# Performance work log

Hardware: AMD Instinct MI355X
Metric: run time of the kernel (lower is better)

## Reference

```python
import jax, jax.numpy as jnp
import numpy as np
from jax import lax

NUM_LAYERS = 4
EPS_BN = 1e-5
EPS_AGG = 1e-6


def _bn(x, gamma, beta):
    # training-mode batch norm over the leading (node/edge) dim
    m = x.mean(axis=0)
    v = x.var(axis=0)
    return gamma * (x - m) / jnp.sqrt(v + EPS_BN) + beta


def setup_inputs() -> dict:
    key = jax.random.key(0)
    ks = jax.random.split(key, 32)
    N, E, D, L, K = 50000, 400000, 64, 128, 16
    s = 0.05
    inp = {
        'reads': jax.random.uniform(ks[0], (N, 4, L), jnp.float32),
        'src': jax.random.randint(ks[1], (E,), 0, N, jnp.int32),
        'dst': jax.random.randint(ks[2], (E,), 0, N, jnp.int32),
        'overlap_similarity': jax.random.uniform(ks[3], (E,), jnp.float32),
        'overlap_length': jax.random.normal(ks[4], (E,), jnp.float32),
        # sequence encoder conv: Conv1d(4 -> D, kernel K)
        'conv_w': jax.random.normal(ks[5], (D, 4, K), jnp.float32) * s,
        'conv_b': jnp.zeros((D,), jnp.float32),
        # edge encoder: Linear(2 -> D)
        'We': jax.random.normal(ks[6], (2, D), jnp.float32) * s,
        'be': jnp.zeros((D,), jnp.float32),
        # GatedGCN per-layer weights, stacked on leading layer dim
        'A1': jax.random.normal(ks[7], (NUM_LAYERS, D, D), jnp.float32) * s,
        'A2': jax.random.normal(ks[8], (NUM_LAYERS, D, D), jnp.float32) * s,
        'A3': jax.random.normal(ks[9], (NUM_LAYERS, D, D), jnp.float32) * s,
        'bA1': jnp.zeros((NUM_LAYERS, D), jnp.float32),
        'bA2': jnp.zeros((NUM_LAYERS, D), jnp.float32),
        'bA3': jnp.zeros((NUM_LAYERS, D), jnp.float32),
        'U': jax.random.normal(ks[10], (NUM_LAYERS, D, D), jnp.float32) * s,
        'V': jax.random.normal(ks[11], (NUM_LAYERS, D, D), jnp.float32) * s,
        'bU': jnp.zeros((NUM_LAYERS, D), jnp.float32),
        'bV': jnp.zeros((NUM_LAYERS, D), jnp.float32),
        'bn_h_gamma': jnp.ones((NUM_LAYERS, D), jnp.float32),
        'bn_h_beta': jnp.zeros((NUM_LAYERS, D), jnp.float32),
        'bn_e_gamma': jnp.ones((NUM_LAYERS, D), jnp.float32),
        'bn_e_beta': jnp.zeros((NUM_LAYERS, D), jnp.float32),
        # edge decoder MLP: Linear(3D -> D) -> ReLU -> Linear(D -> 1)
        'W1': jax.random.normal(ks[12], (3 * D, D), jnp.float32) * s,
        'b1': jnp.zeros((D,), jnp.float32),
        'W2': jax.random.normal(ks[13], (D, 1), jnp.float32) * s,
        'b2': jnp.zeros((1,), jnp.float32),
    }
    return inp


def reference(reads, src, dst, overlap_similarity, overlap_length,
              conv_w, conv_b, We, be,
              A1, A2, A3, bA1, bA2, bA3, U, V, bU, bV,
              bn_h_gamma, bn_h_beta, bn_e_gamma, bn_e_beta,
              W1, b1, W2, b2):
    N = reads.shape[0]
    # --- SequenceEncoder: Conv1d over one-hot reads, global max-pool ---
    hseq = lax.conv_general_dilated(
        reads, conv_w, window_strides=(1,), padding='VALID',
        dimension_numbers=('NCH', 'OIH', 'NCH'))  # [N, D, L-K+1]
    h = (hseq + conv_b[None, :, None]).max(axis=2)  # [N, D]
    # --- EdgeEncoder: Linear on [similarity, length] ---
    e = jnp.stack([overlap_similarity, overlap_length], axis=1) @ We + be  # [E, D]
    # --- stacked GatedGCN layers (gather src/dst, scatter-aggregate to dst) ---
    for l in range(NUM_LAYERS):
        hs = h[src]  # [E, D] gather
        hd = h[dst]
        e_hat = (hs @ A1[l] + bA1[l]) + (hd @ A2[l] + bA2[l]) + (e @ A3[l] + bA3[l])
        sigma = jax.nn.sigmoid(e_hat)  # edge gates
        Vh = hs @ V[l] + bV[l]
        num = jax.ops.segment_sum(sigma * Vh, dst, num_segments=N)  # [N, D]
        den = jax.ops.segment_sum(sigma, dst, num_segments=N)
        h_hat = (h @ U[l] + bU[l]) + num / (den + EPS_AGG)
        h = h + jax.nn.relu(_bn(h_hat, bn_h_gamma[l], bn_h_beta[l]))
        e = e + jax.nn.relu(_bn(e_hat, bn_e_gamma[l], bn_e_beta[l]))
    # --- EdgeDecoder: MLP on [h_src, h_dst, e] ---
    z = jnp.concatenate([h[src], h[dst], e], axis=1)  # [E, 3D]
    p = jax.nn.relu(z @ W1 + b1) @ W2 + b2  # [E, 1]
    return p
```

## Files before the change

### kernel.cpp

```cpp
#include <hip/hip_runtime.h>
#include <hip/hip_bf16.h>
#include <cstdint>
#include <cstddef>

#define DD 64

typedef __attribute__((ext_vector_type(8))) short short8;
typedef __attribute__((ext_vector_type(4))) float f32x4;

__device__ __forceinline__ float4 f4_0() { return make_float4(0.f, 0.f, 0.f, 0.f); }

__device__ __forceinline__ unsigned short f2bf(float f) {
  __hip_bfloat16 h = __float2bfloat16(f);
  return *reinterpret_cast<unsigned short*>(&h);
}
__device__ __forceinline__ float bfl(unsigned u) { return __uint_as_float(u << 16); }
__device__ __forceinline__ float bfh(unsigned u) { return __uint_as_float(u & 0xffff0000u); }
__device__ __forceinline__ float b2f(unsigned short u) {
  return __uint_as_float(((unsigned)u) << 16);
}

__device__ __forceinline__ short8 pack_bf16x8(float4 a, float4 b) {
  union { unsigned short us[8]; short8 v; } pk;
  pk.us[0] = f2bf(a.x); pk.us[1] = f2bf(a.y); pk.us[2] = f2bf(a.z); pk.us[3] = f2bf(a.w);
  pk.us[4] = f2bf(b.x); pk.us[5] = f2bf(b.y); pk.us[6] = f2bf(b.z); pk.us[7] = f2bf(b.w);
  return pk.v;
}

__device__ __forceinline__ short8 lds_frag(const unsigned short* p) {
  uint2 lo = *reinterpret_cast<const uint2*>(p);
  uint2 hi = *reinterpret_cast<const uint2*>(p + 4);
  union { unsigned u[4]; short8 v; } t;
  t.u[0] = lo.x; t.u[1] = lo.y; t.u[2] = hi.x; t.u[3] = hi.y;
  return t.v;
}
__device__ __forceinline__ short8 g_frag(const unsigned short* p) {
  return *reinterpret_cast<const short8*>(p);
}
__device__ __forceinline__ short8 u4_to_s8(uint4 v) {
  union { uint4 u; short8 s; } t; t.u = v; return t.s;
}

__global__ __launch_bounds__(256) void k_hist(const int* __restrict__ dst,
                                              int* __restrict__ cnt, int E) {
  int j = blockIdx.x * 256 + threadIdx.x;
  if (j < E) atomicAdd(&cnt[dst[j]], 1);
}

__global__ __launch_bounds__(1024) void k_scan(const int* __restrict__ cnt,
                                               int* __restrict__ row_ptr,
                                               int* __restrict__ nxt, int N, int E) {
  __shared__ int wsum[16];
  __shared__ int carry_s;
  const int tid = threadIdx.x;
  const int wid = tid >> 6, lane = tid & 63;
  if (tid == 0) carry_s = 0;
  __syncthreads();
  const int ntl = (N + 4095) / 4096;
  for (int b = 0; b < ntl; ++b) {
    const int i0 = b * 4096 + tid * 4;
    int v0 = 0, v1 = 0, v2 = 0, v3 = 0;
    if (i0 + 3 < N) {
      int4 q = *reinterpret_cast<const int4*>(cnt + i0);
      v0 = q.x; v1 = q.y; v2 = q.z; v3 = q.w;
    } else {
      if (i0 < N) v0 = cnt[i0];
      if (i0 + 1 < N) v1 = cnt[i0 + 1];
      if (i0 + 2 < N) v2 = cnt[i0 + 2];
      if (i0 + 3 < N) v3 = cnt[i0 + 3];
    }
    const int tsum = v0 + v1 + v2 + v3;
    int x = tsum;
#pragma unroll
    for (int off = 1; off < 64; off <<= 1) {
      int y = __shfl_up(x, off, 64);
      if (lane >= off) x += y;
    }
    if (lane == 63) wsum[wid] = x;
    __syncthreads();
    if (wid == 0 && lane < 16) {
      int wv = wsum[lane];
#pragma unroll
      for (int off = 1; off < 16; off <<= 1) {
        int y = __shfl_up(wv, off, 64);
        if (lane >= off) wv += y;
      }
      wsum[lane] = wv;
    }
    __syncthreads();
    int base = carry_s + (wid > 0 ? wsum[wid - 1] : 0) + (x - tsum);
    int e1 = base + v0, e2 = e1 + v1, e3 = e2 + v2;
    if (i0 < N) { row_ptr[i0] = base; nxt[i0] = base; }
    if (i0 + 1 < N) { row_ptr[i0 + 1] = e1; nxt[i0 + 1] = e1; }
    if (i0 + 2 < N) { row_ptr[i0 + 2] = e2; nxt[i0 + 2] = e2; }
    if (i0 + 3 < N) { row_ptr[i0 + 3] = e3; nxt[i0 + 3] = e3; }
    __syncthreads();
    if (tid == 0) carry_s += wsum[15];
    __syncthreads();
  }
  if (tid == 0) row_ptr[N] = E;
}

__global__ __launch_bounds__(256) void k_scatter(const int* __restrict__ dst,
                                                 const int* __restrict__ src,
                                                 int* __restrict__ nxt,
                                                 int* __restrict__ order,
                                                 int* __restrict__ psrc,
                                                 int2* __restrict__ pedge, int E) {
  int j = blockIdx.x * 256 + threadIdx.x;
  if (j >= E) return;
  int d = dst[j];
  int s = src[j];
  int pos = atomicAdd(&nxt[d], 1);
  order[pos] = j;
  psrc[pos] = s;
  pedge[pos] = make_int2(s, d);
}

__global__ __launch_bounds__(256) void k_prep(const float* __restrict__ A1,
                                              const float* __restrict__ A2,
                                              const float* __restrict__ V,
                                              const float* __restrict__ U,
                                              const float* __restrict__ A3,
                                              const float* __restrict__ W1,
                                              unsigned short* __restrict__ T) {
  const int b = blockIdx.x;
  const int tid = threadIdx.x;
  if (b < 20) {
    const int l = b / 5, m = b % 5;
    const float* srcp =
        (m == 0 ? A1 : m == 1 ? A2 : m == 2 ? V : m == 3 ? U : A3) + l * 4096;
    unsigned short* dstp = T + b * 4096;
    for (int i = tid; i < 4096; i += 256) {
      int n = i >> 6, k = i & 63;
      dstp[i] = f2bf(srcp[k * 64 + n]);
    }
  } else {
    unsigned short* dstp = T + 20 * 4096;
    for (int i = tid; i < 12288; i += 256) {
      int n = i / 192, k = i % 192;
      dstp[i] = f2bf(W1[k * 64 + n]);
    }
  }
}

struct ConvRegs { float4 v[3][2]; };

__device__ __forceinline__ void conv_load(const float* __restrict__ reads, int N,
                                          int g, int tid, ConvRegs& R) {
#pragma unroll
  for (int it = 0; it < 3; ++it) {
    const int task = tid + it * 256;
    R.v[it][0] = f4_0(); R.v[it][1] = f4_0();
    if (task < 576) {
      const int node = task / 144, rem = task % 144;
      const int c = rem / 36, u = rem % 36;
      const int gn = g * 4 + node;
      if (gn < N) {
        const float* rp = reads + (size_t)gn * 512 + c * 128 + 4 * u;
        if (u <= 31) R.v[it][0] = *reinterpret_cast<const float4*>(rp);
        if (u <= 30) R.v[it][1] = *reinterpret_cast<const float4*>(rp + 4);
      }
    }
  }
}

__device__ __forceinline__ void conv_write(unsigned short* __restrict__ cbuf,
                                           int tid, const ConvRegs& R) {
#pragma unroll
  for (int it = 0; it < 3; ++it) {
    const int task = tid + it * 256;
    if (task < 576) {
      const int node = task / 144, rem = task % 144;
      const int c = rem / 36, u = rem % 36;
      const float4 v0 = R.v[it][0], v1 = R.v[it][1];
      unsigned pk0, pk1, pk2, pk3;
      asm("v_cvt_pk_bf16_f32 %0, %1, %2" : "=v"(pk0) : "v"(v0.x), "v"(v0.y));
      asm("v_cvt_pk_bf16_f32 %0, %1, %2" : "=v"(pk1) : "v"(v0.z), "v"(v0.w));
      asm("v_cvt_pk_bf16_f32 %0, %1, %2" : "=v"(pk2) : "v"(v1.x), "v"(v1.y));
      asm("v_cvt_pk_bf16_f32 %0, %1, %2" : "=v"(pk3) : "v"(v1.z), "v"(v1.w));
      const unsigned a0 = __builtin_amdgcn_alignbit(pk1, pk0, 16);
      const unsigned a1 = __builtin_amdgcn_alignbit(pk2, pk1, 16);
      const unsigned a2 = __builtin_amdgcn_alignbit(pk3, pk2, 16);
      const int base = ((node * 4 + c) * 4) * 144 + 4 * u;
      *reinterpret_cast<uint2*>(&cbuf[base + 0 * 144]) = make_uint2(pk0, pk1);
      *reinterpret_cast<uint2*>(&cbuf[base + 1 * 144]) = make_uint2(a0, a1);
      *reinterpret_cast<uint2*>(&cbuf[base + 2 * 144]) = make_uint2(pk1, pk2);
      *reinterpret_cast<uint2*>(&cbuf[base + 3 * 144]) = make_uint2(a1, a2);
    }
  }
}

__global__ __launch_bounds__(256) void k_conv_mfma(const float* __restrict__ reads,
                                                   const float* __restrict__ w,
                                                   const float* __restrict__ bias,
                                                   float* __restrict__ h, int N) {
  __shared__ unsigned short cp[2][4 * 4 * 4 * 144];
  const int tid = threadIdx.x;
  const int wid = tid >> 6, lane = tid & 63;
  const int col = lane & 15, grp = lane >> 4;
  const int ngroups = (N + 3) / 4;
  if ((int)blockIdx.x >= ngroups) return;
  short8 wf[4][2];
#pragma unroll
  for (int nt = 0; nt < 4; ++nt)
#pragma unroll
    for (int ks = 0; ks < 2; ++ks) {
      const int d = nt * 16 + col;
      const int kb = ks * 32 + grp * 8;
      const float* wp = w + d * 64 + kb;
      float4 w0 = *reinterpret_cast<const float4*>(wp);
      float4 w1 = *reinterpret_cast<const float4*>(wp + 4);
      wf[nt][ks] = pack_bf16x8(w0, w1);
    }
  ConvRegs RA, RB;
  conv_load(reads, N, blockIdx.x, tid, RA);
  int p = 0;
  const int s = col & 3;
  for (int g = blockIdx.x; g < ngroups; g += gridDim.x) {
    conv_write(&cp[p][0], tid, RA);
    const int gnext = g + gridDim.x;
    if (gnext < ngroups) conv_load(reads, N, gnext, tid, RB);
    __syncthreads();
    const int gn = g * 4 + wid;
    if (gn < N) {
      const unsigned short* cbuf = &cp[p][0];
      float vmax[4];
#pragma unroll
      for (int nt = 0; nt < 4; ++nt) vmax[nt] = -3.0e38f;
      for (int mt = 0; mt < 8; ++mt) {
        const int t = mt * 16 + col;
        short8 af[2];
#pragma unroll
        for (int ks = 0; ks < 2; ++ks) {
          const int kbase = ks * 32 + grp * 8;
          const int c = kbase >> 4;
          const int kk0 = kbase & 15;
          const int q = (t - s) + kk0;
          af[ks] = lds_frag(&cbuf[((wid * 4 + c) * 4 + s) * 144 + q]);
        }
        f32x4 acc[4] = {};
#pragma unroll
        for (int ks = 0; ks < 2; ++ks)
#pragma unroll
          for (int nt = 0; nt < 4; ++nt)
            acc[nt] = __builtin_amdgcn_mfma_f32_16x16x32_bf16(af[ks], wf[nt][ks], acc[nt], 0, 0, 0);
        if (mt < 7) {
#pragma unroll
          for (int nt = 0; nt < 4; ++nt)
#pragma unroll
            for (int r = 0; r < 4; ++r) vmax[nt] = fmaxf(vmax[nt], acc[nt][r]);
        } else {
          if (grp == 0) {
#pragma unroll
            for (int nt = 0; nt < 4; ++nt) vmax[nt] = fmaxf(vmax[nt], acc[nt][0]);
          }
        }
      }
#pragma unroll
      for (int off = 16; off <= 32; off <<= 1)
#pragma unroll
        for (int nt = 0; nt < 4; ++nt)
          vmax[nt] = fmaxf(vmax[nt], __shfl_xor(vmax[nt], off, 64));
      if (grp == 0) {
#pragma unroll
        for (int nt = 0; nt < 4; ++nt) {
          const int d = nt * 16 + col;
          h[(size_t)gn * 64 + d] = vmax[nt] + bias[d];
        }
      }
    }
    p ^= 1;
    RA = RB;
  }
}

__global__ __launch_bounds__(256) void k_node_mfma(const float* __restrict__ h_in,
                                                   float* __restrict__ h_out,
                                                   const float* __restrict__ hhat,
                                                   const float* __restrict__ sums_prev,
                                                   const float* __restrict__ gam,
                                                   const float* __restrict__ bet,
                                                   const unsigned short* __restrict__ Wt4,
                                                   const float* __restrict__ bA1,
                                                   const float* __restrict__ bA2,
                                                   const float* __restrict__ bV,
                                                   const float* __restrict__ bU,
                                                   unsigned short* __restrict__ XA1,
                                                   unsigned short* __restrict__ XA2,
                                                   unsigned short* __restrict__ XV,
                                                   float* __restrict__ XU,
                                                   int N, int hasupd) {
  __shared__ float s_coef[128];
  const int tid = threadIdx.x;
  if (hasupd) {
    if (tid < 64) {
      const float invR = 1.f / (float)N;
      float mean = sums_prev[tid] * invR;
      float var = sums_prev[64 + tid] * invR - mean * mean;
      float sc = gam[tid] * rsqrtf(var + 1e-5f);
      s_coef[tid] = sc;
      s_coef[64 + tid] = bet[tid] - mean * sc;
    }
    __syncthreads();
  }
  const int wid = tid >> 6, lane = tid & 63;
  const int col = lane & 15, g = lane >> 4;
  const int ntiles = (N + 15) / 16;
  for (int tw = blockIdx.x * 4 + wid; tw < ntiles; tw += gridDim.x * 4) {
    int n = tw * 16 + col;
    const bool valid = n < N;
    if (!valid) n = N - 1;
    short8 bfr[2];
#pragma unroll
    for (int ks = 0; ks < 2; ++ks) {
      const int c0 = ks * 32 + g * 8;
      const float* hp = h_in + (size_t)n * 64 + c0;
      float4 x0 = *reinterpret_cast<const float4*>(hp);
      float4 x1 = *reinterpret_cast<const float4*>(hp + 4);
      if (hasupd) {
        const float* yp = hhat + (size_t)n * 64 + c0;
        float4 y0 = *reinterpret_cast<const float4*>(yp);
        float4 y1 = *reinterpret_cast<const float4*>(yp + 4);
        float4 sc0 = *reinterpret_cast<const float4*>(&s_coef[c0]);
        float4 sc1 = *reinterpret_cast<const float4*>(&s_coef[c0 + 4]);
        float4 sh0 = *reinterpret_cast<const float4*>(&s_coef[64 + c0]);
        float4 sh1 = *reinterpret_cast<const float4*>(&s_coef[64 + c0 + 4]);
        x0.x += fmaxf(fmaf(sc0.x, y0.x, sh0.x), 0.f);
        x0.y += fmaxf(fmaf(sc0.y, y0.y, sh0.y), 0.f);
        x0.z += fmaxf(fmaf(sc0.z, y0.z, sh0.z), 0.f);
        x0.w += fmaxf(fmaf(sc0.w, y0.w, sh0.w), 0.f);
        x1.x += fmaxf(fmaf(sc1.x, y1.x, sh1.x), 0.f);
        x1.y += fmaxf(fmaf(sc1.y, y1.y, sh1.y), 0.f);
        x1.z += fmaxf(fmaf(sc1.z, y1.z, sh1.z), 0.f);
        x1.w += fmaxf(fmaf(sc1.w, y1.w, sh1.w), 0.f);
        if (valid) {
          float* op = h_out + (size_t)n * 64 + c0;
          *reinterpret_cast<float4*>(op) = x0;
          *reinterpret_cast<float4*>(op + 4) = x1;
        }
      }
      bfr[ks] = pack_bf16x8(x0, x1);
    }
#pragma unroll
    for (int m = 0; m < 4; ++m) {
      const unsigned short* Wm = Wt4 + m * 4096;
      f32x4 acc[4] = {};
#pragma unroll
      for (int ks = 0; ks < 2; ++ks) {
        const int ko = ks * 32 + g * 8;
#pragma unroll
        for (int mt = 0; mt < 4; ++mt) {
          short8 aa = g_frag(Wm + (mt * 16 + col) * 64 + ko);
          acc[mt] = __builtin_amdgcn_mfma_f32_16x16x32_bf16(aa, bfr[ks], acc[mt], 0, 0, 0);
        }
      }
      if (!valid) continue;
      const float* bb = (m == 0) ? bA1 : (m == 1) ? bA2 : (m == 2) ? bV : bU;
#pragma unroll
      for (int mt = 0; mt < 4; ++mt) {
        const int chb = mt * 16 + g * 4;
        float4 bv = *reinterpret_cast<const float4*>(bb + chb);
        float o0 = acc[mt][0] + bv.x;
        float o1 = acc[mt][1] + bv.y;
        float o2 = acc[mt][2] + bv.z;
        float o3 = acc[mt][3] + bv.w;
        if (m < 3) {
          unsigned short* X = (m == 0) ? XA1 : (m == 1) ? XA2 : XV;
          ushort4 ov;
          ov.x = f2bf(o0); ov.y = f2bf(o1); ov.z = f2bf(o2); ov.w = f2bf(o3);
          *reinterpret_cast<ushort4*>(X + (size_t)n * 64 + chb) = ov;
        } else {
          *reinterpret_cast<float4*>(XU + (size_t)n * 64 + chb) =
              make_float4(o0, o1, o2, o3);
        }
      }
    }
  }
}

__global__ __launch_bounds__(256) void k_edge_mfma0(unsigned short* __restrict__ e,
                                                    unsigned short* __restrict__ ehat_out,
                                                    const float* __restrict__ sim,
                                                    const float* __restrict__ olen,
                                                    const int* __restrict__ order,
                                                    const float* __restrict__ We,
                                                    const float* __restrict__ be,
                                                    const int2* __restrict__ pedge,
                                                    const unsigned short* __restrict__ XA1,
                                                    const unsigned short* __restrict__ XA2,
                                                    const unsigned short* __restrict__ A3t,
                                                    const float* __restrict__ bA3,
                                                    float* __restrict__ sums_out, int E) {
  __shared__ float s_sums[128];
  const int tid = threadIdx.x;
  if (tid < 128) s_sums[tid] = 0.f;
  __syncthreads();
  const int wid = tid >> 6, lane = tid & 63;
  const int col = lane & 15, g = lane >> 4;
  float4 ba[4];
#pragma unroll
  for (int mt = 0; mt < 4; ++mt)
    ba[mt] = *reinterpret_cast<const float4*>(bA3 + mt * 16 + g * 4);
  float4 w0[2][2], w1[2][2], bev[2][2];
#pragma unroll
  for (int ks = 0; ks < 2; ++ks) {
    const int c0 = ks * 32 + g * 8;
    w0[ks][0] = *reinterpret_cast<const float4*>(We + c0);
    w0[ks][1] = *reinterpret_cast<const float4*>(We + c0 + 4);
    w1[ks][0] = *reinterpret_cast<const float4*>(We + 64 + c0);
    w1[ks][1] = *reinterpret_cast<const float4*>(We + 64 + c0 + 4);
    bev[ks][0] = *reinterpret_cast<const float4*>(be + c0);
    bev[ks][1] = *reinterpret_cast<const float4*>(be + c0 + 4);
  }
  float statS[16], statQ[16];
#pragma unroll
  for (int i = 0; i < 16; ++i) { statS[i] = 0.f; statQ[i] = 0.f; }
  const int ntiles = (E + 15) / 16;
  const int stride = gridDim.x * 4;
  int tw = blockIdx.x * 4 + wid;
  int2 idx_n = make_int2(0, 0);
  int oe_n = 0;
  if (tw < ntiles) {
    int p = tw * 16 + col; if (p >= E) p = E - 1;
    idx_n = pedge[p];
    oe_n = order[p];
  }
  for (; tw < ntiles; tw += stride) {
    int p = tw * 16 + col;
    const bool valid = p < E;
    if (!valid) p = E - 1;
    const int se = idx_n.x, de = idx_n.y;
    const float sv = sim[oe_n], lv = olen[oe_n];
    ushort4 gx1[4], gx2[4];
#pragma unroll
    for (int mt = 0; mt < 4; ++mt) {
      const int chb = mt * 16 + g * 4;
      gx1[mt] = *reinterpret_cast<const ushort4*>(XA1 + (size_t)se * 64 + chb);
      gx2[mt] = *reinterpret_cast<const ushort4*>(XA2 + (size_t)de * 64 + chb);
    }
    const int twn = tw + stride;
    if (twn < ntiles) {
      int pn = twn * 16 + col; if (pn >= E) pn = E - 1;
      idx_n = pedge[pn];
      oe_n = order[pn];
    }
    short8 bfr[2];
#pragma unroll
    for (int ks = 0; ks < 2; ++ks) {
      float4 e0, e1;
      e0.x = fmaf(sv, w0[ks][0].x, fmaf(lv, w1[ks][0].x, bev[ks][0].x));
      e0.y = fmaf(sv, w0[ks][0].y, fmaf(lv, w1[ks][0].y, bev[ks][0].y));
      e0.z = fmaf(sv, w0[ks][0].z, fmaf(lv, w1[ks][0].z, bev[ks][0].z));
      e0.w = fmaf(sv, w0[ks][0].w, fmaf(lv, w1[ks][0].w, bev[ks][0].w));
      e1.x = fmaf(sv, w0[ks][1].x, fmaf(lv, w1[ks][1].x, bev[ks][1].x));
      e1.y = fmaf(sv, w0[ks][1].y, fmaf(lv, w1[ks][1].y, bev[ks][1].y));
      e1.z = fmaf(sv, w0[ks][1].z, fmaf(lv, w1[ks][1].z, bev[ks][1].z));
      e1.w = fmaf(sv, w0[ks][1].w, fmaf(lv, w1[ks][1].w, bev[ks][1].w));
      bfr[ks] = pack_bf16x8(e0, e1);
      if (valid)
        *reinterpret_cast<short8*>(e + (size_t)p * 64 + ks * 32 + g * 8) = bfr[ks];
    }
    f32x4 acc[4] = {};
#pragma unroll
    for (int ks = 0; ks < 2; ++ks)
#pragma unroll
      for (int mt = 0; mt < 4; ++mt) {
        short8 aa = g_frag(A3t + (mt * 16 + col) * 64 + ks * 32 + g * 8);
        acc[mt] = __builtin_amdgcn_mfma_f32_16x16x32_bf16(aa, bfr[ks], acc[mt], 0, 0, 0);
      }
    if (valid) {
#pragma unroll
      for (int mt = 0; mt < 4; ++mt) {
        const int chb = mt * 16 + g * 4;
        float o0 = acc[mt][0] + b2f(gx1[mt].x) + b2f(gx2[mt].x) + ba[mt].x;
        float o1 = acc[mt][1] + b2f(gx1[mt].y) + b2f(gx2[mt].y) + ba[mt].y;
        float o2 = acc[mt][2] + b2f(gx1[mt].z) + b2f(gx2[mt].z) + ba[mt].z;
        float o3 = acc[mt][3] + b2f(gx1[mt].w) + b2f(gx2[mt].w) + ba[mt].w;
        ushort4 ov;
        ov.x = f2bf(o0); ov.y = f2bf(o1); ov.z = f2bf(o2); ov.w = f2bf(o3);
        *reinterpret_cast<ushort4*>(ehat_out + (size_t)p * 64 + chb) = ov;
        statS[mt * 4 + 0] += o0; statQ[mt * 4 + 0] = fmaf(o0, o0, statQ[mt * 4 + 0]);
        statS[mt * 4 + 1] += o1; statQ[mt * 4 + 1] = fmaf(o1, o1, statQ[mt * 4 + 1]);
        statS[mt * 4 + 2] += o2; statQ[mt * 4 + 2] = fmaf(o2, o2, statQ[mt * 4 + 2]);
        statS[mt * 4 + 3] += o3; statQ[mt * 4 + 3] = fmaf(o3, o3, statQ[mt * 4 + 3]);
      }
    }
  }
#pragma unroll
  for (int off = 1; off <= 8; off <<= 1)
#pragma unroll
    for (int i = 0; i < 16; ++i) {
      statS[i] += __shfl_xor(statS[i], off, 64);
      statQ[i] += __shfl_xor(statQ[i], off, 64);
    }
  if (col == 0) {
#pragma unroll
    for (int mt = 0; mt < 4; ++mt)
#pragma unroll
      for (int c = 0; c < 4; ++c) {
        const int ch = mt * 16 + g * 4 + c;
        atomicAdd(&s_sums[ch], statS[mt * 4 + c]);
        atomicAdd(&s_sums[64 + ch], statQ[mt * 4 + c]);
      }
  }
  __syncthreads();
  if (tid < 128) atomicAdd(&sums_out[tid], s_sums[tid]);
}

__global__ __launch_bounds__(256) void k_edge_mfma(unsigned short* __restrict__ e,
                                                   const unsigned short* __restrict__ ehat_prev,
                                                   unsigned short* __restrict__ ehat_out,
                                                   const float* __restrict__ sums_prev,
                                                   const float* __restrict__ gprev,
                                                   const float* __restrict__ bprev,
                                                   const int2* __restrict__ pedge,
                                                   const unsigned short* __restrict__ XA1,
                                                   const unsigned short* __restrict__ XA2,
                                                   const unsigned short* __restrict__ A3t,
                                                   const float* __restrict__ bA3,
                                                   float* __restrict__ sums_out, int E) {
  __shared__ float s_coef[128];
  __shared__ float s_sums[128];
  const int tid = threadIdx.x;
  if (tid < 128) s_sums[tid] = 0.f;
  if (tid < 64) {
    float mean = sums_prev[tid] / (float)E;
    float var = sums_prev[64 + tid] / (float)E - mean * mean;
    float sc = gprev[tid] * rsqrtf(var + 1e-5f);
    s_coef[tid] = sc;
    s_coef[64 + tid] = bprev[tid] - mean * sc;
  }
  __syncthreads();
  const int wid = tid >> 6, lane = tid & 63;
  const int col = lane & 15, g = lane >> 4;
  float4 ba[4];
#pragma unroll
  for (int mt = 0; mt < 4; ++mt)
    ba[mt] = *reinterpret_cast<const float4*>(bA3 + mt * 16 + g * 4);
  float statS[16], statQ[16];
#pragma unroll
  for (int i = 0; i < 16; ++i) { statS[i] = 0.f; statQ[i] = 0.f; }
  const int ntiles = (E + 15) / 16;
  const int stride = gridDim.x * 4;
  int tw = blockIdx.x * 4 + wid;
  int2 idx_n = make_int2(0, 0);
  uint4 eo_n0, eo_n1, hv_n0, hv_n1;
  if (tw < ntiles) {
    int p = tw * 16 + col; if (p >= E) p = E - 1;
    idx_n = pedge[p];
    const unsigned short* ep = e + (size_t)p * 64 + g * 8;
    eo_n0 = *reinterpret_cast<const uint4*>(ep);
    eo_n1 = *reinterpret_cast<const uint4*>(ep + 32);
    const unsigned short* hp = ehat_prev + (size_t)p * 64 + g * 8;
    hv_n0 = *reinterpret_cast<const uint4*>(hp);
    hv_n1 = *reinterpret_cast<const uint4*>(hp + 32);
  }
  for (; tw < ntiles; tw += stride) {
    int p = tw * 16 + col;
    const bool valid = p < E;
    if (!valid) p = E - 1;
    const int se = idx_n.x, de = idx_n.y;
    const uint4 eoc[2] = {eo_n0, eo_n1};
    const uint4 hvc[2] = {hv_n0, hv_n1};
    ushort4 gx1[4], gx2[4];
#pragma unroll
    for (int mt = 0; mt < 4; ++mt) {
      const int chb = mt * 16 + g * 4;
      gx1[mt] = *reinterpret_cast<const ushort4*>(XA1 + (size_t)se * 64 + chb);
      gx2[mt] = *reinterpret_cast<const ushort4*>(XA2 + (size_t)de * 64 + chb);
    }
    const int twn = tw + stride;
    if (twn < ntiles) {
      int pn = twn * 16 + col; if (pn >= E) pn = E - 1;
      idx_n = pedge[pn];
      const unsigned short* ep = e + (size_t)pn * 64 + g * 8;
      eo_n0 = *reinterpret_cast<const uint4*>(ep);
      eo_n1 = *reinterpret_cast<const uint4*>(ep + 32);
      const unsigned short* hp = ehat_prev + (size_t)pn * 64 + g * 8;
      hv_n0 = *reinterpret_cast<const uint4*>(hp);
      hv_n1 = *reinterpret_cast<const uint4*>(hp + 32);
    }
    short8 bfr[2];
#pragma unroll
    for (int ks = 0; ks < 2; ++ks) {
      const int c0 = ks * 32 + g * 8;
      const uint4 eo = eoc[ks];
      const uint4 hv = hvc[ks];
      float4 e0 = make_float4(bfl(eo.x), bfh(eo.x), bfl(eo.y), bfh(eo.y));
      float4 e1 = make_float4(bfl(eo.z), bfh(eo.z), bfl(eo.w), bfh(eo.w));
      float4 sc0 = *reinterpret_cast<const float4*>(&s_coef[c0]);
      float4 sc1 = *reinterpret_cast<const float4*>(&s_coef[c0 + 4]);
      float4 sh0 = *reinterpret_cast<const float4*>(&s_coef[64 + c0]);
      float4 sh1 = *reinterpret_cast<const float4*>(&s_coef[64 + c0 + 4]);
      e0.x += fmaxf(fmaf(sc0.x, bfl(hv.x), sh0.x), 0.f);
      e0.y += fmaxf(fmaf(sc0.y, bfh(hv.x), sh0.y), 0.f);
      e0.z += fmaxf(fmaf(sc0.z, bfl(hv.y), sh0.z), 0.f);
      e0.w += fmaxf(fmaf(sc0.w, bfh(hv.y), sh0.w), 0.f);
      e1.x += fmaxf(fmaf(sc1.x, bfl(hv.z), sh1.x), 0.f);
      e1.y += fmaxf(fmaf(sc1.y, bfh(hv.z), sh1.y), 0.f);
      e1.z += fmaxf(fmaf(sc1.z, bfl(hv.w), sh1.z), 0.f);
      e1.w += fmaxf(fmaf(sc1.w, bfh(hv.w), sh1.w), 0.f);
      bfr[ks] = pack_bf16x8(e0, e1);
      if (valid)
        *reinterpret_cast<short8*>(e + (size_t)p * 64 + c0) = bfr[ks];
    }
    f32x4 acc[4] = {};
#pragma unroll
    for (int ks = 0; ks < 2; ++ks)
#pragma unroll
      for (int mt = 0; mt < 4; ++mt) {
        short8 aa = g_frag(A3t + (mt * 16 + col) * 64 + ks * 32 + g * 8);
        acc[mt] = __builtin_amdgcn_mfma_f32_16x16x32_bf16(aa, bfr[ks], acc[mt], 0, 0, 0);
      }
    if (valid) {
#pragma unroll
      for (int mt = 0; mt < 4; ++mt) {
        const int chb = mt * 16 + g * 4;
        float o0 = acc[mt][0] + b2f(gx1[mt].x) + b2f(gx2[mt].x) + ba[mt].x;
        float o1 = acc[mt][1] + b2f(gx1[mt].y) + b2f(gx2[mt].y) + ba[mt].y;
        float o2 = acc[mt][2] + b2f(gx1[mt].z) + b2f(gx2[mt].z) + ba[mt].z;
        float o3 = acc[mt][3] + b2f(gx1[mt].w) + b2f(gx2[mt].w) + ba[mt].w;
        ushort4 ov;
        ov.x = f2bf(o0); ov.y = f2bf(o1); ov.z = f2bf(o2); ov.w = f2bf(o3);
        *reinterpret_cast<ushort4*>(ehat_out + (size_t)p * 64 + chb) = ov;
        statS[mt * 4 + 0] += o0; statQ[mt * 4 + 0] = fmaf(o0, o0, statQ[mt * 4 + 0]);
        statS[mt * 4 + 1] += o1; statQ[mt * 4 + 1] = fmaf(o1, o1, statQ[mt * 4 + 1]);
        statS[mt * 4 + 2] += o2; statQ[mt * 4 + 2] = fmaf(o2, o2, statQ[mt * 4 + 2]);
        statS[mt * 4 + 3] += o3; statQ[mt * 4 + 3] = fmaf(o3, o3, statQ[mt * 4 + 3]);
      }
    }
  }
#pragma unroll
  for (int off = 1; off <= 8; off <<= 1)
#pragma unroll
    for (int i = 0; i < 16; ++i) {
      statS[i] += __shfl_xor(statS[i], off, 64);
      statQ[i] += __shfl_xor(statQ[i], off, 64);
    }
  if (col == 0) {
#pragma unroll
    for (int mt = 0; mt < 4; ++mt)
#pragma unroll
      for (int c = 0; c < 4; ++c) {
        const int ch = mt * 16 + g * 4 + c;
        atomicAdd(&s_sums[ch], statS[mt * 4 + c]);
        atomicAdd(&s_sums[64 + ch], statQ[mt * 4 + c]);
      }
  }
  __syncthreads();
  if (tid < 128) atomicAdd(&sums_out[tid], s_sums[tid]);
}

__global__ __launch_bounds__(256) void k_agg(const int* __restrict__ row_ptr,
                                             const int* __restrict__ psrc,
                                             const unsigned short* __restrict__ ehat,
                                             const unsigned short* __restrict__ XV,
                                             const float* __restrict__ XU,
                                             float* __restrict__ hhat,
                                             float* __restrict__ sums_h, int N) {
  __shared__ float s_sums[128];
  const int tid = threadIdx.x;
  if (tid < 128) s_sums[tid] = 0.f;
  __syncthreads();
  float sS[4] = {0.f, 0.f, 0.f, 0.f}, sQ[4] = {0.f, 0.f, 0.f, 0.f};
  const int total = N * 16;
  for (int idx = blockIdx.x * 256 + tid; idx < total; idx += gridDim.x * 256) {
    int n = idx >> 4, dc = (idx & 15) << 2;
    int beg = row_ptr[n], end = row_ptr[n + 1];
    float4 nm = f4_0(), dn = f4_0();
    for (int i = beg; i < end; ++i) {
      int sj = psrc[i];
      uint2 ev = *reinterpret_cast<const uint2*>(ehat + (size_t)i * 64 + dc);
      uint2 vv = *reinterpret_cast<const uint2*>(XV + (size_t)sj * 64 + dc);
      float s0 = 1.f / (1.f + __expf(-bfl(ev.x)));
      float s1 = 1.f / (1.f + __expf(-bfh(ev.x)));
      float s2 = 1.f / (1.f + __expf(-bfl(ev.y)));
      float s3 = 1.f / (1.f + __expf(-bfh(ev.y)));
      dn.x += s0; dn.y += s1; dn.z += s2; dn.w += s3;
      nm.x = fmaf(s0, bfl(vv.x), nm.x);
      nm.y = fmaf(s1, bfh(vv.x), nm.y);
      nm.z = fmaf(s2, bfl(vv.y), nm.z);
      nm.w = fmaf(s3, bfh(vv.y), nm.w);
    }
    float4 xu = *reinterpret_cast<const float4*>(XU + (size_t)n * 64 + dc);
    float h0 = xu.x + nm.x / (dn.x + 1e-6f);
    float h1 = xu.y + nm.y / (dn.y + 1e-6f);
    float h2 = xu.z + nm.z / (dn.z + 1e-6f);
    float h3 = xu.w + nm.w / (dn.w + 1e-6f);
    *reinterpret_cast<float4*>(hhat + (size_t)n * 64 + dc) = make_float4(h0, h1, h2, h3);
    sS[0] += h0; sQ[0] = fmaf(h0, h0, sQ[0]);
    sS[1] += h1; sQ[1] = fmaf(h1, h1, sQ[1]);
    sS[2] += h2; sQ[2] = fmaf(h2, h2, sQ[2]);
    sS[3] += h3; sQ[3] = fmaf(h3, h3, sQ[3]);
  }
#pragma unroll
  for (int off = 16; off <= 32; off <<= 1)
#pragma unroll
    for (int c = 0; c < 4; ++c) {
      sS[c] += __shfl_xor(sS[c], off, 64);
      sQ[c] += __shfl_xor(sQ[c], off, 64);
    }
  const int lane = tid & 63;
  if (lane < 16) {
    const int dc = lane << 2;
#pragma unroll
    for (int c = 0; c < 4; ++c) {
      atomicAdd(&s_sums[dc + c], sS[c]);
      atomicAdd(&s_sums[64 + dc + c], sQ[c]);
    }
  }
  __syncthreads();
  if (tid < 128) atomicAdd(&sums_h[tid], s_sums[tid]);
}

__global__ __launch_bounds__(256) void k_update_h(float* __restrict__ h,
                                                  unsigned short* __restrict__ hb,
                                                  const float* __restrict__ hhat,
                                                  const float* __restrict__ sums,
                                                  const float* __restrict__ gamma,
                                                  const float* __restrict__ beta, int R) {
  int idx = blockIdx.x * 256 + threadIdx.x;
  if (idx >= R * 16) return;
  int r = idx >> 4, dc = (idx & 15) << 2;
  const float invR = 1.f / (float)R;
  float4 sv = *reinterpret_cast<const float4*>(sums + dc);
  float4 qv = *reinterpret_cast<const float4*>(sums + 64 + dc);
  float4 gm = *reinterpret_cast<const float4*>(gamma + dc);
  float4 bt = *reinterpret_cast<const float4*>(beta + dc);
  float m0 = sv.x * invR, m1 = sv.y * invR, m2 = sv.z * invR, m3 = sv.w * invR;
  float c0 = gm.x * rsqrtf(qv.x * invR - m0 * m0 + 1e-5f);
  float c1 = gm.y * rsqrtf(qv.y * invR - m1 * m1 + 1e-5f);
  float c2 = gm.z * rsqrtf(qv.z * invR - m2 * m2 + 1e-5f);
  float c3 = gm.w * rsqrtf(qv.w * invR - m3 * m3 + 1e-5f);
  float h0 = bt.x - m0 * c0, h1 = bt.y - m1 * c1, h2 = bt.z - m2 * c2, h3 = bt.w - m3 * c3;
  size_t off = (size_t)r * 64 + dc;
  float4 y = *reinterpret_cast<const float4*>(hhat + off);
  float4 x = *reinterpret_cast<const float4*>(h + off);
  x.x += fmaxf(fmaf(c0, y.x, h0), 0.f);
  x.y += fmaxf(fmaf(c1, y.y, h1), 0.f);
  x.z += fmaxf(fmaf(c2, y.z, h2), 0.f);
  x.w += fmaxf(fmaf(c3, y.w, h3), 0.f);
  *reinterpret_cast<float4*>(h + off) = x;
  ushort4 hv;
  hv.x = f2bf(x.x); hv.y = f2bf(x.y); hv.z = f2bf(x.z); hv.w = f2bf(x.w);
  *reinterpret_cast<ushort4*>(hb + off) = hv;
}

__global__ __launch_bounds__(256) void k_decoder_mfma(const unsigned short* __restrict__ hb,
                                                      const unsigned short* __restrict__ e,
                                                      const unsigned short* __restrict__ ehat3,
                                                      const float* __restrict__ sums_e3,
                                                      const float* __restrict__ ge3,
                                                      const float* __restrict__ be3,
                                                      const int2* __restrict__ pedge,
                                                      const int* __restrict__ order,
                                                      const unsigned short* __restrict__ W1t,
                                                      const float* __restrict__ b1,
                                                      const float* __restrict__ W2,
                                                      const float* __restrict__ b2,
                                                      float* __restrict__ out, int E) {
  __shared__ unsigned short Wt[64 * 200];
  __shared__ float s_coef[128];
  const int tid = threadIdx.x;
  if (tid < 64) {
    float mean = sums_e3[tid] / (float)E;
    float var = sums_e3[64 + tid] / (float)E - mean * mean;
    float sc = ge3[tid] * rsqrtf(var + 1e-5f);
    s_coef[tid] = sc;
    s_coef[64 + tid] = be3[tid] - mean * sc;
  }
  for (int i = tid; i < 1536; i += 256) {
    int n = i / 24, kc = (i % 24) * 8;
    *reinterpret_cast<uint4*>(&Wt[n * 200 + kc]) =
        *reinterpret_cast<const uint4*>(W1t + n * 192 + kc);
  }
  __syncthreads();
  const int wid = tid >> 6, lane = tid & 63;
  const int col = lane & 15, g = lane >> 4;
  float b1v[4], w2v[4];
#pragma unroll
  for (int nt = 0; nt < 4; ++nt) { b1v[nt] = b1[nt * 16 + col]; w2v[nt] = W2[nt * 16 + col]; }
  const float bb2 = b2[0];
  const int ntiles = (E + 15) / 16;
  const int stride = gridDim.x * 4;
  int tw = blockIdx.x * 4 + wid;
  int2 idx_n = make_int2(0, 0);
  uint4 eo_n0, eo_n1, hv_n0, hv_n1;
  if (tw < ntiles) {
    int p = tw * 16 + col; if (p >= E) p = E - 1;
    idx_n = pedge[p];
    const unsigned short* ep = e + (size_t)p * 64 + g * 8;
    eo_n0 = *reinterpret_cast<const uint4*>(ep);
    eo_n1 = *reinterpret_cast<const uint4*>(ep + 32);
    const unsigned short* hp = ehat3 + (size_t)p * 64 + g * 8;
    hv_n0 = *reinterpret_cast<const uint4*>(hp);
    hv_n1 = *reinterpret_cast<const uint4*>(hp + 32);
  }
  for (; tw < ntiles; tw += stride) {
    const int eb = tw * 16;
    int p = eb + col;
    const bool valid = p < E;
    if (!valid) p = E - 1;
    const int se = idx_n.x, de = idx_n.y;
    const uint4 eoc[2] = {eo_n0, eo_n1};
    const uint4 hvc[2] = {hv_n0, hv_n1};
    short8 haf[4];
#pragma unroll
    for (int ks = 0; ks < 4; ++ks) {
      const unsigned short* hp = hb + (size_t)(ks < 2 ? se : de) * 64 + (ks & 1) * 32 + g * 8;
      haf[ks] = g_frag(hp);
    }
    const int twn = tw + stride;
    if (twn < ntiles) {
      int pn = twn * 16 + col; if (pn >= E) pn = E - 1;
      idx_n = pedge[pn];
      const unsigned short* ep = e + (size_t)pn * 64 + g * 8;
      eo_n0 = *reinterpret_cast<const uint4*>(ep);
      eo_n1 = *reinterpret_cast<const uint4*>(ep + 32);
      const unsigned short* hp = ehat3 + (size_t)pn * 64 + g * 8;
      hv_n0 = *reinterpret_cast<const uint4*>(hp);
      hv_n1 = *reinterpret_cast<const uint4*>(hp + 32);
    }
    f32x4 acc[4] = {};
#pragma unroll
    for (int ks = 0; ks < 6; ++ks) {
      short8 af;
      if (ks < 4) {
        af = haf[ks];
      } else {
        const int kse = ks - 4;
        const int c0 = kse * 32 + g * 8;
        const uint4 eo = eoc[kse];
        const uint4 hv = hvc[kse];
        float4 a0 = make_float4(bfl(eo.x), bfh(eo.x), bfl(eo.y), bfh(eo.y));
        float4 a1 = make_float4(bfl(eo.z), bfh(eo.z), bfl(eo.w), bfh(eo.w));
        float4 sc0 = *reinterpret_cast<const float4*>(&s_coef[c0]);
        float4 sc1 = *reinterpret_cast<const float4*>(&s_coef[c0 + 4]);
        float4 sh0 = *reinterpret_cast<const float4*>(&s_coef[64 + c0]);
        float4 sh1 = *reinterpret_cast<const float4*>(&s_coef[64 + c0 + 4]);
        a0.x += fmaxf(fmaf(sc0.x, bfl(hv.x), sh0.x), 0.f);
        a0.y += fmaxf(fmaf(sc0.y, bfh(hv.x), sh0.y), 0.f);
        a0.z += fmaxf(fmaf(sc0.z, bfl(hv.y), sh0.z), 0.f);
        a0.w += fmaxf(fmaf(sc0.w, bfh(hv.y), sh0.w), 0.f);
        a1.x += fmaxf(fmaf(sc1.x, bfl(hv.z), sh1.x), 0.f);
        a1.y += fmaxf(fmaf(sc1.y, bfh(hv.z), sh1.y), 0.f);
        a1.z += fmaxf(fmaf(sc1.z, bfl(hv.w), sh1.z), 0.f);
        a1.w += fmaxf(fmaf(sc1.w, bfh(hv.w), sh1.w), 0.f);
        af = pack_bf16x8(a0, a1);
      }
#pragma unroll
      for (int nt = 0; nt < 4; ++nt) {
        short8 bb = lds_frag(&Wt[(nt * 16 + col) * 200 + ks * 32 + g * 8]);
        acc[nt] = __builtin_amdgcn_mfma_f32_16x16x32_bf16(af, bb, acc[nt], 0, 0, 0);
      }
    }
    float pr[4];
#pragma unroll
    for (int r = 0; r < 4; ++r) {
      float s = 0.f;
#pragma unroll
      for (int nt = 0; nt < 4; ++nt)
        s = fmaf(fmaxf(acc[nt][r] + b1v[nt], 0.f), w2v[nt], s);
      pr[r] = s;
    }
#pragma unroll
    for (int off = 1; off <= 8; off <<= 1)
#pragma unroll
      for (int r = 0; r < 4; ++r)
        pr[r] += __shfl_xor(pr[r], off, 64);
    if (col == 0) {
#pragma unroll
      for (int r = 0; r < 4; ++r) {
        int m = eb + g * 4 + r;
        if (m < E) out[order[m]] = pr[r] + bb2;
      }
    }
  }
}

extern "C" void kernel_launch(void* const* d_in, const int* in_sizes, int n_in,
                              void* d_out, int out_size, void* d_ws, size_t ws_size,
                              hipStream_t stream) {
  const float* reads  = (const float*)d_in[0];
  const int*   src    = (const int*)d_in[1];
  const int*   dst    = (const int*)d_in[2];
  const float* sim    = (const float*)d_in[3];
  const float* olen   = (const float*)d_in[4];
  const float* conv_w = (const float*)d_in[5];
  const float* conv_b = (const float*)d_in[6];
  const float* We     = (const float*)d_in[7];
  const float* be     = (const float*)d_in[8];
  const float* A1     = (const float*)d_in[9];
  const float* A2     = (const float*)d_in[10];
  const float* A3     = (const float*)d_in[11];
  const float* bA1    = (const float*)d_in[12];
  const float* bA2    = (const float*)d_in[13];
  const float* bA3    = (const float*)d_in[14];
  const float* U      = (const float*)d_in[15];
  const float* V      = (const float*)d_in[16];
  const float* bU     = (const float*)d_in[17];
  const float* bV     = (const float*)d_in[18];
  const float* bnhg   = (const float*)d_in[19];
  const float* bnhb   = (const float*)d_in[20];
  const float* bneg   = (const float*)d_in[21];
  const float* bneb   = (const float*)d_in[22];
  const float* W1     = (const float*)d_in[23];
  const float* b1     = (const float*)d_in[24];
  const float* W2     = (const float*)d_in[25];
  const float* b2     = (const float*)d_in[26];

  const int N = in_sizes[0] / 512;
  const int E = in_sizes[1];

  float* fp = (float*)d_ws;
  float* hA   = fp; fp += (size_t)N * 64;
  float* hB   = fp; fp += (size_t)N * 64;
  float* hhat = fp; fp += (size_t)N * 64;
  float* XU   = fp; fp += (size_t)N * 64;
  float* sums = fp; fp += 1024;
  unsigned short* up = (unsigned short*)fp;
  unsigned short* e     = up; up += (size_t)E * 64;
  unsigned short* ehatA = up; up += (size_t)E * 64;
  unsigned short* ehatB = up; up += (size_t)E * 64;
  unsigned short* XA1 = up; up += (size_t)N * 64;
  unsigned short* XA2 = up; up += (size_t)N * 64;
  unsigned short* XV  = up; up += (size_t)N * 64;
  unsigned short* hb  = up; up += (size_t)N * 64;
  unsigned short* Wt  = up; up += 20 * 4096 + 12288;
  int* ip = (int*)up;
  int* order   = ip; ip += E;
  int* psrc    = ip; ip += E;
  int2* pedge  = (int2*)ip; ip += 2 * (size_t)E;
  int* cnt     = ip; ip += N;
  int* nxt     = ip; ip += N;
  int* row_ptr = ip; ip += N + 1;
  float* out = (float*)d_out;

  hipMemsetAsync(cnt, 0, sizeof(int) * N, stream);
  hipMemsetAsync(sums, 0, sizeof(float) * 1024, stream);
  k_hist<<<(E + 255) / 256, 256, 0, stream>>>(dst, cnt, E);
  k_prep<<<21, 256, 0, stream>>>(A1, A2, V, U, A3, W1, Wt);
  k_scan<<<1, 1024, 0, stream>>>(cnt, row_ptr, nxt, N, E);
  k_scatter<<<(E + 255) / 256, 256, 0, stream>>>(dst, src, nxt, order, psrc, pedge, E);

  const int ngroups = (N + 3) / 4;
  const int CG = ngroups < 1024 ? ngroups : 1024;
  k_conv_mfma<<<CG, 256, 0, stream>>>(reads, conv_w, conv_b, hA, N);

  const int EPBLK = 1024;
  const int APBLK = 1024;
  const int NPB = 512;
  float* hin = hA;
  float* hout = hB;
  unsigned short* ehat_cur = ehatA;
  unsigned short* ehat_prev = ehatB;
  for (int l = 0; l < 4; ++l) {
    ehat_cur = (l & 1) ? ehatB : ehatA;
    ehat_prev = (l & 1) ? ehatA : ehatB;
    float* sums_e = sums + l * 128;
    float* sums_h = sums + 512 + l * 128;
    k_node_mfma<<<NPB, 256, 0, stream>>>(
        hin, (l > 0) ? hout : nullptr, hhat,
        (l > 0) ? (sums + 512 + (l - 1) * 128) : sums,
        bnhg + (l > 0 ? (l - 1) * 64 : 0), bnhb + (l > 0 ? (l - 1) * 64 : 0),
        Wt + l * 5 * 4096,
        bA1 + l * 64, bA2 + l * 64, bV + l * 64, bU + l * 64,
        XA1, XA2, XV, XU, N, l > 0 ? 1 : 0);
    if (l > 0) { float* t = hin; hin = hout; hout = t; }
    if (l == 0) {
      k_edge_mfma0<<<EPBLK, 256, 0, stream>>>(
          e, ehat_cur, sim, olen, order, We, be, pedge, XA1, XA2,
          Wt + 4 * 4096, bA3, sums_e, E);
    } else {
      k_edge_mfma<<<EPBLK, 256, 0, stream>>>(
          e, ehat_prev, ehat_cur, sums + (l - 1) * 128,
          bneg + (l - 1) * 64, bneb + (l - 1) * 64,
          pedge, XA1, XA2, Wt + (l * 5 + 4) * 4096, bA3 + l * 64, sums_e, E);
    }
    k_agg<<<APBLK, 256, 0, stream>>>(row_ptr, psrc, ehat_cur, XV, XU, hhat, sums_h, N);
  }

  k_update_h<<<(N * 16 + 255) / 256, 256, 0, stream>>>(
      hin, hb, hhat, sums + 512 + 3 * 128, bnhg + 3 * 64, bnhb + 3 * 64, N);
  k_decoder_mfma<<<EPBLK, 256, 0, stream>>>(
      hb, e, ehat_cur, sums + 3 * 128, bneg + 3 * 64, bneb + 3 * 64,
      pedge, order, Wt + 20 * 4096, b1, W2, b2, out, E);
}
```

Baseline: 768.6 us.

## Halve conv LDS staging, chunk edge/aggregate loops contiguously with XCD-aware block mapping

The conv staging buffer now stores only two shifted bf16 copies per channel instead of four; odd shifts of 2 and 3 are served by dword-offset reads from the existing copies, so the kernel loads fewer reads and does less LDS writing. The edge, aggregate and decoder kernels switch from grid-stride loops to contiguous per-wave tile chunks, and remap block IDs so that blocks placed on the same XCD (round-robin across 8) process neighbouring ranges, which is meant to improve L2 locality for the dst-sorted edges. The conv grid size also doubles. Risks include load imbalance from the static chunking and the assumption that gridDim is a multiple of 8.

```diff
diff --git a/kernel.cpp b/kernel.cpp
--- a/kernel.cpp
+++ b/kernel.cpp
@@ -36,9 +36,6 @@
 }
 __device__ __forceinline__ short8 g_frag(const unsigned short* p) {
   return *reinterpret_cast<const short8*>(p);
-}
-__device__ __forceinline__ short8 u4_to_s8(uint4 v) {
-  union { uint4 u; short8 s; } t; t.u = v; return t.s;
 }
 
 __global__ __launch_bounds__(256) void k_hist(const int* __restrict__ dst,
@@ -144,22 +141,22 @@
   }
 }
 
-struct ConvRegs { float4 v[3][2]; };
+struct ConvRegs { float4 a[3]; float2 b[3]; };
 
 __device__ __forceinline__ void conv_load(const float* __restrict__ reads, int N,
                                           int g, int tid, ConvRegs& R) {
 #pragma unroll
   for (int it = 0; it < 3; ++it) {
     const int task = tid + it * 256;
-    R.v[it][0] = f4_0(); R.v[it][1] = f4_0();
+    R.a[it] = f4_0(); R.b[it] = make_float2(0.f, 0.f);
     if (task < 576) {
       const int node = task / 144, rem = task % 144;
       const int c = rem / 36, u = rem % 36;
       const int gn = g * 4 + node;
       if (gn < N) {
         const float* rp = reads + (size_t)gn * 512 + c * 128 + 4 * u;
-        if (u <= 31) R.v[it][0] = *reinterpret_cast<const float4*>(rp);
-        if (u <= 30) R.v[it][1] = *reinterpret_cast<const float4*>(rp + 4);
+        if (u <= 31) R.a[it] = *reinterpret_cast<const float4*>(rp);
+        if (u <= 30) R.b[it] = *reinterpret_cast<const float2*>(rp + 4);
       }
     }
   }
@@ -173,20 +170,17 @@
     if (task < 576) {
       const int node = task / 144, rem = task % 144;
       const int c = rem / 36, u = rem % 36;
-      const float4 v0 = R.v[it][0], v1 = R.v[it][1];
-      unsigned pk0, pk1, pk2, pk3;
+      const float4 v0 = R.a[it];
+      const float2 v1 = R.b[it];
+      unsigned pk0, pk1, pk2;
       asm("v_cvt_pk_bf16_f32 %0, %1, %2" : "=v"(pk0) : "v"(v0.x), "v"(v0.y));
       asm("v_cvt_pk_bf16_f32 %0, %1, %2" : "=v"(pk1) : "v"(v0.z), "v"(v0.w));
       asm("v_cvt_pk_bf16_f32 %0, %1, %2" : "=v"(pk2) : "v"(v1.x), "v"(v1.y));
-      asm("v_cvt_pk_bf16_f32 %0, %1, %2" : "=v"(pk3) : "v"(v1.z), "v"(v1.w));
       const unsigned a0 = __builtin_amdgcn_alignbit(pk1, pk0, 16);
       const unsigned a1 = __builtin_amdgcn_alignbit(pk2, pk1, 16);
-      const unsigned a2 = __builtin_amdgcn_alignbit(pk3, pk2, 16);
-      const int base = ((node * 4 + c) * 4) * 144 + 4 * u;
-      *reinterpret_cast<uint2*>(&cbuf[base + 0 * 144]) = make_uint2(pk0, pk1);
-      *reinterpret_cast<uint2*>(&cbuf[base + 1 * 144]) = make_uint2(a0, a1);
-      *reinterpret_cast<uint2*>(&cbuf[base + 2 * 144]) = make_uint2(pk1, pk2);
-      *reinterpret_cast<uint2*>(&cbuf[base + 3 * 144]) = make_uint2(a1, a2);
+      const int base = ((node * 4 + c) * 2) * 144 + 4 * u;
+      *reinterpret_cast<uint2*>(&cbuf[base]) = make_uint2(pk0, pk1);
+      *reinterpret_cast<uint2*>(&cbuf[base + 144]) = make_uint2(a0, a1);
     }
   }
 }
@@ -195,7 +189,7 @@
                                                    const float* __restrict__ w,
                                                    const float* __restrict__ bias,
                                                    float* __restrict__ h, int N) {
-  __shared__ unsigned short cp[2][4 * 4 * 4 * 144];
+  __shared__ unsigned short cp[2][4 * 4 * 2 * 144];
   const int tid = threadIdx.x;
   const int wid = tid >> 6, lane = tid & 63;
   const int col = lane & 15, grp = lane >> 4;
@@ -217,6 +211,8 @@
   conv_load(reads, N, blockIdx.x, tid, RA);
   int p = 0;
   const int s = col & 3;
+  const int scpy = s & 1;
+  const bool shi = s >= 2;
   for (int g = blockIdx.x; g < ngroups; g += gridDim.x) {
     conv_write(&cp[p][0], tid, RA);
     const int gnext = g + gridDim.x;
@@ -237,7 +233,17 @@
           const int c = kbase >> 4;
           const int kk0 = kbase & 15;
           const int q = (t - s) + kk0;
-          af[ks] = lds_frag(&cbuf[((wid * 4 + c) * 4 + s) * 144 + q]);
+          const unsigned short* base = &cbuf[((wid * 4 + c) * 2 + scpy) * 144];
+          if (!shi) {
+            af[ks] = lds_frag(base + q);
+          } else {
+            const unsigned* p32 = reinterpret_cast<const unsigned*>(base);
+            const int d0 = (q >> 1) + 1;
+            union { unsigned u[4]; short8 v; } t2;
+            t2.u[0] = p32[d0]; t2.u[1] = p32[d0 + 1];
+            t2.u[2] = p32[d0 + 2]; t2.u[3] = p32[d0 + 3];
+            af[ks] = t2.v;
+          }
         }
         f32x4 acc[4] = {};
 #pragma unroll
@@ -416,17 +422,21 @@
   float statS[16], statQ[16];
 #pragma unroll
   for (int i = 0; i < 16; ++i) { statS[i] = 0.f; statQ[i] = 0.f; }
+  const int X8 = gridDim.x >> 3;
+  const int vb = (blockIdx.x & 7) * X8 + (blockIdx.x >> 3);
   const int ntiles = (E + 15) / 16;
-  const int stride = gridDim.x * 4;
-  int tw = blockIdx.x * 4 + wid;
+  const int nw = gridDim.x * 4;
+  const int chunk = (ntiles + nw - 1) / nw;
+  int tw = (vb * 4 + wid) * chunk;
+  int tw_end = tw + chunk; if (tw_end > ntiles) tw_end = ntiles;
   int2 idx_n = make_int2(0, 0);
   int oe_n = 0;
-  if (tw < ntiles) {
+  if (tw < tw_end) {
     int p = tw * 16 + col; if (p >= E) p = E - 1;
     idx_n = pedge[p];
     oe_n = order[p];
   }
-  for (; tw < ntiles; tw += stride) {
+  for (; tw < tw_end; ++tw) {
     int p = tw * 16 + col;
     const bool valid = p < E;
     if (!valid) p = E - 1;
@@ -439,8 +449,8 @@
       gx1[mt] = *reinterpret_cast<const ushort4*>(XA1 + (size_t)se * 64 + chb);
       gx2[mt] = *reinterpret_cast<const ushort4*>(XA2 + (size_t)de * 64 + chb);
     }
-    const int twn = tw + stride;
-    if (twn < ntiles) {
+    const int twn = tw + 1;
+    if (twn < tw_end) {
       int pn = twn * 16 + col; if (pn >= E) pn = E - 1;
       idx_n = pedge[pn];
       oe_n = order[pn];
@@ -541,12 +551,16 @@
   float statS[16], statQ[16];
 #pragma unroll
   for (int i = 0; i < 16; ++i) { statS[i] = 0.f; statQ[i] = 0.f; }
+  const int X8 = gridDim.x >> 3;
+  const int vb = (blockIdx.x & 7) * X8 + (blockIdx.x >> 3);
   const int ntiles = (E + 15) / 16;
-  const int stride = gridDim.x * 4;
-  int tw = blockIdx.x * 4 + wid;
+  const int nw = gridDim.x * 4;
+  const int chunk = (ntiles + nw - 1) / nw;
+  int tw = (vb * 4 + wid) * chunk;
+  int tw_end = tw + chunk; if (tw_end > ntiles) tw_end = ntiles;
   int2 idx_n = make_int2(0, 0);
-  uint4 eo_n0, eo_n1, hv_n0, hv_n1;
-  if (tw < ntiles) {
+  uint4 eo_n0 = {}, eo_n1 = {}, hv_n0 = {}, hv_n1 = {};
+  if (tw < tw_end) {
     int p = tw * 16 + col; if (p >= E) p = E - 1;
     idx_n = pedge[p];
     const unsigned short* ep = e + (size_t)p * 64 + g * 8;
@@ -556,7 +570,7 @@
     hv_n0 = *reinterpret_cast<const uint4*>(hp);
     hv_n1 = *reinterpret_cast<const uint4*>(hp + 32);
   }
-  for (; tw < ntiles; tw += stride) {
+  for (; tw < tw_end; ++tw) {
     int p = tw * 16 + col;
     const bool valid = p < E;
     if (!valid) p = E - 1;
@@ -570,8 +584,8 @@
       gx1[mt] = *reinterpret_cast<const ushort4*>(XA1 + (size_t)se * 64 + chb);
       gx2[mt] = *reinterpret_cast<const ushort4*>(XA2 + (size_t)de * 64 + chb);
     }
-    const int twn = tw + stride;
-    if (twn < ntiles) {
+    const int twn = tw + 1;
+    if (twn < tw_end) {
       int pn = twn * 16 + col; if (pn >= E) pn = E - 1;
       idx_n = pedge[pn];
       const unsigned short* ep = e + (size_t)pn * 64 + g * 8;
@@ -664,8 +678,14 @@
   if (tid < 128) s_sums[tid] = 0.f;
   __syncthreads();
   float sS[4] = {0.f, 0.f, 0.f, 0.f}, sQ[4] = {0.f, 0.f, 0.f, 0.f};
+  const int X8 = gridDim.x >> 3;
+  const int vb = (blockIdx.x & 7) * X8 + (blockIdx.x >> 3);
   const int total = N * 16;
-  for (int idx = blockIdx.x * 256 + tid; idx < total; idx += gridDim.x * 256) {
+  const int per = (int)(gridDim.x * 256);
+  const int chunk = (total + per - 1) / per;
+  for (int it = 0; it < chunk; ++it) {
+    const int idx = (vb * chunk + it) * 256 + tid;
+    if (idx >= total) continue;
     int n = idx >> 4, dc = (idx & 15) << 2;
     int beg = row_ptr[n], end = row_ptr[n + 1];
     float4 nm = f4_0(), dn = f4_0();
@@ -782,12 +802,16 @@
 #pragma unroll
   for (int nt = 0; nt < 4; ++nt) { b1v[nt] = b1[nt * 16 + col]; w2v[nt] = W2[nt * 16 + col]; }
   const float bb2 = b2[0];
+  const int X8 = gridDim.x >> 3;
+  const int vb = (blockIdx.x & 7) * X8 + (blockIdx.x >> 3);
   const int ntiles = (E + 15) / 16;
-  const int stride = gridDim.x * 4;
-  int tw = blockIdx.x * 4 + wid;
+  const int nw = gridDim.x * 4;
+  const int chunk = (ntiles + nw - 1) / nw;
+  int tw = (vb * 4 + wid) * chunk;
+  int tw_end = tw + chunk; if (tw_end > ntiles) tw_end = ntiles;
   int2 idx_n = make_int2(0, 0);
-  uint4 eo_n0, eo_n1, hv_n0, hv_n1;
-  if (tw < ntiles) {
+  uint4 eo_n0 = {}, eo_n1 = {}, hv_n0 = {}, hv_n1 = {};
+  if (tw < tw_end) {
     int p = tw * 16 + col; if (p >= E) p = E - 1;
     idx_n = pedge[p];
     const unsigned short* ep = e + (size_t)p * 64 + g * 8;
@@ -797,7 +821,7 @@
     hv_n0 = *reinterpret_cast<const uint4*>(hp);
     hv_n1 = *reinterpret_cast<const uint4*>(hp + 32);
   }
-  for (; tw < ntiles; tw += stride) {
+  for (; tw < tw_end; ++tw) {
     const int eb = tw * 16;
     int p = eb + col;
     const bool valid = p < E;
@@ -811,8 +835,8 @@
       const unsigned short* hp = hb + (size_t)(ks < 2 ? se : de) * 64 + (ks & 1) * 32 + g * 8;
       haf[ks] = g_frag(hp);
     }
-    const int twn = tw + stride;
-    if (twn < ntiles) {
+    const int twn = tw + 1;
+    if (twn < tw_end) {
       int pn = twn * 16 + col; if (pn >= E) pn = E - 1;
       idx_n = pedge[pn];
       const unsigned short* ep = e + (size_t)pn * 64 + g * 8;
@@ -945,7 +969,7 @@
   k_scatter<<<(E + 255) / 256, 256, 0, stream>>>(dst, src, nxt, order, psrc, pedge, E);
 
   const int ngroups = (N + 3) / 4;
-  const int CG = ngroups < 1024 ? ngroups : 1024;
+  const int CG = ngroups < 2048 ? ngroups : 2048;
   k_conv_mfma<<<CG, 256, 0, stream>>>(reads, conv_w, conv_b, hA, N);
 
   const int EPBLK = 1024;
```

New measurement: 860.2 us. 1.12x slower.
